# Performance work log

Hardware: AMD Instinct MI355X
Metric: run time of the kernel (lower is better)

Reference implementation:

```python
import jax, jax.numpy as jnp
import numpy as np

V = 32000      # vocab_size
CHI = 64       # bond_dim
PD = 64        # pos_dim
MAXLEN = 1024  # max_seq_len
B, T = 8, 512
LN_EPS = 1e-5


def setup_inputs() -> dict:
    key = jax.random.key(0)
    ks = jax.random.split(key, 8)
    return {
        "input_ids": jax.random.randint(ks[0], (B, T), 0, V),
        "target_ids": jax.random.randint(ks[1], (B, T), 0, V),
        # learned parameters (match torch init scales)
        "core": jax.random.normal(ks[2], (CHI, V, CHI), jnp.float32) * (1.0 / np.sqrt(CHI)),
        "h0": jax.random.normal(ks[3], (CHI,), jnp.float32) * 0.01,
        "pos_embed": jax.random.normal(ks[4], (MAXLEN, PD), jnp.float32) * 0.02,
        # mod_mlp: Linear(PD, 2*PD) -> GELU -> Linear(2*PD, 2*CHI), xavier gain=0.1, zero bias
        "W1": jax.random.normal(ks[5], (PD, 2 * PD), jnp.float32) * (0.1 * np.sqrt(6.0 / (PD + 2 * PD)) / np.sqrt(3.0)),
        "b1": jnp.zeros((2 * PD,), jnp.float32),
        "W2": jax.random.normal(ks[6], (2 * PD, 2 * CHI), jnp.float32) * (0.1 * np.sqrt(6.0 / (2 * PD + 2 * CHI)) / np.sqrt(3.0)),
        "b2": jnp.zeros((2 * CHI,), jnp.float32),
        "output_bias": jnp.zeros((V,), jnp.float32),
        "ln_gamma": jnp.ones((CHI,), jnp.float32),
        "ln_beta": jnp.zeros((CHI,), jnp.float32),
    }


def reference(input_ids, target_ids, core, h0, pos_embed, W1, b1, W2, b2,
              output_bias, ln_gamma, ln_beta):
    Bb, Tt = input_ids.shape
    chi = core.shape[0]

    # position modulation factors for positions 0..T-1
    pos_emb = pos_embed[:Tt]                                  # (T, PD)
    hmid = jax.nn.gelu(pos_emb @ W1 + b1, approximate=False)  # (T, 2*PD)
    mod = hmid @ W2 + b2                                      # (T, 2*CHI)
    ml, mr = jnp.split(mod, 2, axis=-1)
    ml = 1.0 + 0.5 * jnp.tanh(ml)                             # (T, chi)
    mr = 1.0 + 0.5 * jnp.tanh(mr)                             # (T, chi)

    def layer_norm(x):
        mu = jnp.mean(x, axis=-1, keepdims=True)
        var = jnp.var(x, axis=-1, keepdims=True)
        return (x - mu) * jax.lax.rsqrt(var + LN_EPS) * ln_gamma + ln_beta

    def step(h, xs):
        ml_t, mr_t, x_t = xs                                   # (chi,), (chi,), (B,)
        h_mod = h * ml_t                                       # (B, chi)
        # logits_t[b,v] = sum_ij h_mod[b,i] core[i,v,j] mr[j]
        core_r = jnp.einsum('ivj,j->iv', core, mr_t)           # (chi, V)
        logits_t = h_mod @ core_r + output_bias                # (B, V)
        # transition: h_new[b,j] = sum_i h_mod[b,i] core[i,x_b,j] mr[j]
        slices = core[:, x_t, :].transpose(1, 0, 2)            # (B, chi, chi)
        h_new = jnp.einsum('bi,bij->bj', h_mod, slices) * mr_t
        h_new = layer_norm(h_new)
        return h_new, logits_t

    h_init = jnp.broadcast_to(h0, (Bb, chi))
    _, logits = jax.lax.scan(step, h_init, (ml, mr, input_ids.T))  # (T, B, V)

    logits = logits.transpose(1, 0, 2).reshape(-1, logits.shape[-1]).astype(jnp.float32)
    targets = target_ids.reshape(-1)
    logp = jax.nn.log_softmax(logits, axis=-1)
    loss = -jnp.mean(jnp.take_along_axis(logp, targets[:, None], axis=1))
    return loss
```

## Files before the change

### kernel.cpp

```cpp
#include <hip/hip_runtime.h>
#include <math.h>

#define V 32000
#define T 512
#define NB 8
#define LN_EPS 1e-5f

typedef __attribute__((ext_vector_type(8))) short short8;
typedef __attribute__((ext_vector_type(4))) float f32x4;

__device__ __forceinline__ unsigned short f2b(float x) {
    unsigned int u = __float_as_uint(x);
    unsigned int r = (u + 0x7fffu + ((u >> 16) & 1u)) >> 16;
    return (unsigned short)r;
}
__device__ __forceinline__ float b2f(unsigned short h) {
    return __uint_as_float(((unsigned int)h) << 16);
}
__device__ __forceinline__ unsigned int pack_rn(float a, float b) {
    unsigned int ua = __float_as_uint(a) + 0x8000u;
    unsigned int ub = __float_as_uint(b) + 0x8000u;
    return __builtin_amdgcn_perm(ub, ua, 0x07060302u);
}

__global__ void k_mod(const float* __restrict__ pos, const float* __restrict__ W1,
                      const float* __restrict__ b1, const float* __restrict__ W2,
                      const float* __restrict__ b2, float* __restrict__ ml,
                      float* __restrict__ mr, unsigned short* __restrict__ mrb) {
    int t = blockIdx.x, tid = threadIdx.x;
    __shared__ float pos_s[64];
    __shared__ float hm_s[128];
    if (tid < 64) pos_s[tid] = pos[t * 64 + tid];
    __syncthreads();
    float acc = b1[tid];
#pragma unroll
    for (int p = 0; p < 64; p++) acc += pos_s[p] * W1[p * 128 + tid];
    float g = acc * 0.5f * (1.0f + erff(acc * 0.70710678118654752f));
    hm_s[tid] = g;
    __syncthreads();
    float acc2 = b2[tid];
#pragma unroll
    for (int k = 0; k < 128; k++) acc2 += hm_s[k] * W2[k * 128 + tid];
    float val = 1.0f + 0.5f * tanhf(acc2);
    if (tid < 64) ml[t * 64 + tid] = val;
    else { int c = tid - 64; mr[t * 64 + c] = val; mrb[t * 64 + c] = f2b(val); }
}

__global__ void __launch_bounds__(256) k_gather(const int* __restrict__ ids,
                                                const float* __restrict__ core,
                                                unsigned int* __restrict__ g) {
    int bt = blockIdx.x;
    int b = bt >> 9, t = bt & 511;
    int x = ids[b * T + t];
    unsigned int* dst = g + (size_t)bt * 2048;
#pragma unroll
    for (int e = 0; e < 2; e++) {
        int k = (e * 256 + threadIdx.x) * 4;
        int i2 = k >> 6, j = k & 63;
        f32x4 a = *reinterpret_cast<const f32x4*>(core + ((size_t)(2 * i2) * V + x) * 64 + j);
        f32x4 c = *reinterpret_cast<const f32x4*>(core + ((size_t)(2 * i2 + 1) * V + x) * 64 + j);
        uint4 o;
        o.x = pack_rn(a.x, c.x);
        o.y = pack_rn(a.y, c.y);
        o.z = pack_rn(a.z, c.z);
        o.w = pack_rn(a.w, c.w);
        *reinterpret_cast<uint4*>(dst + k) = o;
    }
}

__global__ void __launch_bounds__(64) k_scan(
    const unsigned int* __restrict__ g, const float* __restrict__ h0,
    const float* __restrict__ ml, const float* __restrict__ mr,
    const float* __restrict__ gam, const float* __restrict__ bet,
    unsigned short* __restrict__ hmod) {
    const int b = blockIdx.x, j = threadIdx.x;
    __shared__ float hm_s[64];
    float h = h0[j];
    const float gj = gam[j], bj = bet[j];
    const unsigned int* gb = g + (size_t)b * (512 * 2048);
    unsigned int B0[32], B1[32], B2[32], B3[32];
#pragma unroll
    for (int i = 0; i < 32; i++) B0[i] = gb[i * 64 + j];
#pragma unroll
    for (int i = 0; i < 32; i++) B1[i] = gb[2048 + i * 64 + j];

#define SCAN_BODY(TT, USE, PF)                                                \
    {                                                                         \
        int tp = (TT) + 2; if (tp > T - 1) tp = T - 1;                        \
        const unsigned int* gp = gb + (size_t)tp * 2048;                      \
        _Pragma("unroll")                                                     \
        for (int i = 0; i < 32; i++) PF[i] = gp[i * 64 + j];                  \
        float hmj = h * ml[(TT) * 64 + j];                                    \
        hmod[((TT) * 8 + b) * 64 + j] = f2b(hmj);                             \
        hm_s[j] = hmj;                                                        \
        asm volatile("s_waitcnt lgkmcnt(0)" ::: "memory");                    \
        float s0a = 0.f, s1a = 0.f, s0b = 0.f, s1b = 0.f;                     \
        _Pragma("unroll")                                                     \
        for (int i = 0; i < 16; i++) {                                        \
            unsigned int u = USE[i];                                          \
            s0a += __uint_as_float(u << 16) * hm_s[2 * i];                    \
            s1a += __uint_as_float(u & 0xffff0000u) * hm_s[2 * i + 1];        \
        }                                                                     \
        _Pragma("unroll")                                                     \
        for (int i = 16; i < 32; i++) {                                       \
            unsigned int u = USE[i];                                          \
            s0b += __uint_as_float(u << 16) * hm_s[2 * i];                    \
            s1b += __uint_as_float(u & 0xffff0000u) * hm_s[2 * i + 1];        \
        }                                                                     \
        float y = ((s0a + s0b) + (s1a + s1b)) * mr[(TT) * 64 + j];            \
        float sum = y, sq = y * y;                                            \
        _Pragma("unroll")                                                     \
        for (int m = 1; m < 64; m <<= 1) {                                    \
            sum += __shfl_xor(sum, m, 64);                                    \
            sq  += __shfl_xor(sq, m, 64);                                     \
        }                                                                     \
        float mu = sum * (1.f / 64.f);                                        \
        float var = sq * (1.f / 64.f) - mu * mu;                              \
        h = (y - mu) * rsqrtf(var + LN_EPS) * gj + bj;                        \
    }

    for (int t = 0; t < T; t += 4) {
        SCAN_BODY(t, B0, B2)
        SCAN_BODY(t + 1, B1, B3)
        SCAN_BODY(t + 2, B2, B0)
        SCAN_BODY(t + 3, B3, B1)
    }
#undef SCAN_BODY
}

#define BAR_LDS() do {                                             \
        asm volatile("s_waitcnt lgkmcnt(0)" ::: "memory");         \
        __builtin_amdgcn_s_barrier();                              \
    } while (0)

__global__ void __launch_bounds__(512, 4) k_logits(
    const float* __restrict__ core, const unsigned short* __restrict__ mrb,
    const unsigned short* __restrict__ hmod, const float* __restrict__ obias,
    const int* __restrict__ tgt, unsigned int* __restrict__ ws_ms,
    float* __restrict__ ws_tgt) {
    __shared__ __attribute__((aligned(16))) unsigned short r3s[8 * 2312];

    const int tid = threadIdx.x;
    const int w = tid >> 6;
    const int lane = tid & 63;
    const int q = lane >> 4;
    const int l15 = lane & 15;
    const int bx = blockIdx.x;
    const int v0 = bx * 8;
    const int myv = v0 + w;

    short8 cf[8];
#pragma unroll
    for (int it = 0; it < 4; it++) {
        const float* p = core + (((size_t)(it * 16 + l15)) * V + myv) * 64;
#pragma unroll
        for (int ks = 0; ks < 2; ks++) {
            f32x4 x0 = *reinterpret_cast<const f32x4*>(p + ks * 32 + q * 8);
            f32x4 x1 = *reinterpret_cast<const f32x4*>(p + ks * 32 + q * 8 + 4);
            union { short8 s; unsigned int u[4]; } pk;
            pk.u[0] = pack_rn(x0.x, x0.y);
            pk.u[1] = pack_rn(x0.z, x0.w);
            pk.u[2] = pack_rn(x1.x, x1.y);
            pk.u[3] = pack_rn(x1.z, x1.w);
            cf[it * 2 + ks] = pk.s;
        }
    }
    float biasv[4];
#pragma unroll
    for (int r = 0; r < 4; r++) biasv[r] = obias[v0 + (q & 1) * 4 + r];

    for (int ch = 0; ch < 16; ch++) {
        const int t0 = ch * 32;
#pragma unroll
        for (int tt = 0; tt < 2; tt++) {
            const int trow = t0 + tt * 16 + l15;
            short8 mf0 = *reinterpret_cast<const short8*>(mrb + trow * 64 + q * 8);
            short8 mf1 = *reinterpret_cast<const short8*>(mrb + trow * 64 + 32 + q * 8);
#pragma unroll
            for (int it = 0; it < 4; it++) {
                f32x4 acc = {0.f, 0.f, 0.f, 0.f};
                acc = __builtin_amdgcn_mfma_f32_16x16x32_bf16(cf[it * 2], mf0, acc, 0, 0, 0);
                acc = __builtin_amdgcn_mfma_f32_16x16x32_bf16(cf[it * 2 + 1], mf1, acc, 0, 0, 0);
                uint2 dd;
                dd.x = pack_rn(acc.x, acc.y);
                dd.y = pack_rn(acc.z, acc.w);
                *reinterpret_cast<uint2*>(
                    &r3s[w * 2312 + (tt * 16 + l15) * 72 + it * 16 + q * 4]) = dd;
            }
        }
        BAR_LDS();
        const int bb = l15 & 7;
        const int vp = (l15 & 7) * 2312;
#pragma unroll
        for (int e = 0; e < 4; e++) {
            const int tl = w * 4 + e;
            const int t = t0 + tl;
            short8 ra0 = *reinterpret_cast<const short8*>(&r3s[vp + tl * 72 + q * 8]);
            short8 ra1 = *reinterpret_cast<const short8*>(&r3s[vp + tl * 72 + 32 + q * 8]);
            short8 hb0 = *reinterpret_cast<const short8*>(hmod + ((size_t)t * 8 + bb) * 64 + q * 8);
            short8 hb1 = *reinterpret_cast<const short8*>(hmod + ((size_t)t * 8 + bb) * 64 + 32 + q * 8);
            f32x4 acc = {0.f, 0.f, 0.f, 0.f};
            acc = __builtin_amdgcn_mfma_f32_16x16x32_bf16(ra0, hb0, acc, 0, 0, 0);
            acc = __builtin_amdgcn_mfma_f32_16x16x32_bf16(ra1, hb1, acc, 0, 0, 0);
            float vals[4];
#pragma unroll
            for (int r = 0; r < 4; r++) vals[r] = acc[r] + biasv[r];
            if (q < 2 && l15 < 8) {
                int tg = tgt[bb * T + t];
#pragma unroll
                for (int r = 0; r < 4; r++)
                    if (tg == v0 + q * 4 + r) ws_tgt[l15 * T + t] = vals[r];
            }
            float m4 = fmaxf(fmaxf(vals[0], vals[1]), fmaxf(vals[2], vals[3]));
            float s4 = __expf(vals[0] - m4) + __expf(vals[1] - m4) +
                       __expf(vals[2] - m4) + __expf(vals[3] - m4);
            float om = __shfl_xor(m4, 16, 64);
            float os = __shfl_xor(s4, 16, 64);
            float mm = fmaxf(m4, om);
            float mq = b2f(f2b(mm));
            float ss = s4 * __expf(m4 - mq) + os * __expf(om - mq);
            if (q == 0 && l15 < 8) {
                ws_ms[(size_t)bx * 4096 + l15 * T + t] =
                    ((unsigned int)f2b(mq) << 16) | f2b(ss);
            }
        }
        BAR_LDS();
    }
}

__global__ void k_red1(const unsigned int* __restrict__ ws_ms,
                       float* __restrict__ o_m, float* __restrict__ o_s) {
    int bt = blockIdx.x * 256 + threadIdx.x;
    int kg = blockIdx.y;
    float m = -1e30f, s = 0.f;
    for (int kk = 0; kk < 100; kk++) {
        unsigned int pp = ws_ms[(size_t)(kg * 100 + kk) * 4096 + bt];
        float mk = b2f((unsigned short)(pp >> 16));
        float sk = b2f((unsigned short)(pp & 0xffff));
        float m2 = fmaxf(m, mk);
        s = s * __expf(m - m2) + sk * __expf(mk - m2);
        m = m2;
    }
    o_m[kg * 4096 + bt] = m; o_s[kg * 4096 + bt] = s;
}

__global__ void k_red2(const float* __restrict__ o_m, const float* __restrict__ o_s,
                       const float* __restrict__ wtgt, float* __restrict__ out) {
    int bt = blockIdx.x * 256 + threadIdx.x;
    float m = -1e30f, s = 0.f;
    for (int kg = 0; kg < 40; kg++) {
        float mk = o_m[kg * 4096 + bt], sk = o_s[kg * 4096 + bt];
        float m2 = fmaxf(m, mk);
        s = s * __expf(m - m2) + sk * __expf(mk - m2);
        m = m2;
    }
    float term = m + logf(s) - wtgt[bt];
    __shared__ float red[256];
    red[threadIdx.x] = term;
    __syncthreads();
    for (int st = 128; st > 0; st >>= 1) {
        if (threadIdx.x < st) red[threadIdx.x] += red[threadIdx.x + st];
        __syncthreads();
    }
    if (threadIdx.x == 0) atomicAdd(out, red[0] * (1.f / 4096.f));
}

extern "C" void kernel_launch(void* const* d_in, const int* in_sizes, int n_in,
                              void* d_out, int out_size, void* d_ws, size_t ws_size,
                              hipStream_t stream) {
    const int*   ids   = (const int*)d_in[0];
    const int*   tgt   = (const int*)d_in[1];
    const float* core  = (const float*)d_in[2];
    const float* h0    = (const float*)d_in[3];
    const float* pos   = (const float*)d_in[4];
    const float* W1    = (const float*)d_in[5];
    const float* b1    = (const float*)d_in[6];
    const float* W2    = (const float*)d_in[7];
    const float* b2    = (const float*)d_in[8];
    const float* obias = (const float*)d_in[9];
    const float* gam   = (const float*)d_in[10];
    const float* bet   = (const float*)d_in[11];

    char* ws = (char*)d_ws;
    float*          ws_ml  = (float*)(ws + 0);
    float*          ws_mr  = (float*)(ws + 131072);
    unsigned short* ws_mrb = (unsigned short*)(ws + 262144);
    unsigned short* ws_hm  = (unsigned short*)(ws + 327680);
    float*          ws_tg  = (float*)(ws + 851968);
    unsigned int*   g      = (unsigned int*)(ws + 868352);
    unsigned int*   ws_ms  = (unsigned int*)(ws + 868352);
    float*          o2m    = (float*)(ws + 66404352);
    float*          o2s    = (float*)(ws + 67059712);

    hipMemsetAsync(d_out, 0, sizeof(float), stream);

    k_mod<<<512, 128, 0, stream>>>(pos, W1, b1, W2, b2, ws_ml, ws_mr, ws_mrb);
    k_gather<<<4096, 256, 0, stream>>>(ids, core, g);
    k_scan<<<NB, 64, 0, stream>>>(g, h0, ws_ml, ws_mr, gam, bet, ws_hm);
    k_logits<<<4000, 512, 0, stream>>>(core, ws_mrb, ws_hm, obias, tgt, ws_ms, ws_tg);
    k_red1<<<dim3(16, 40), 256, 0, stream>>>(ws_ms, o2m, o2s);
    k_red2<<<16, 256, 0, stream>>>(o2m, o2s, ws_tg, (float*)d_out);
}
```

Before: 1.948 ms.

## Double-buffer LDS in logits kernel and use all lanes in second-stage MFMA

Splits the shared-memory staging buffer into two halves so that the first MFMA stage for the next 32-timestep chunk can run while the second stage consumes the previous chunk, cutting one barrier per chunk. The second stage is also remapped so the upper half of each 16-lane group handles a second timestep, halving the per-wave MFMA iterations from four to two. This doubles LDS use per block, which may reduce occupancy at 4 blocks per CU.

```diff
diff --git a/kernel.cpp b/kernel.cpp
--- a/kernel.cpp
+++ b/kernel.cpp
@@ -138,7 +138,7 @@
     const unsigned short* __restrict__ hmod, const float* __restrict__ obias,
     const int* __restrict__ tgt, unsigned int* __restrict__ ws_ms,
     float* __restrict__ ws_tgt) {
-    __shared__ __attribute__((aligned(16))) unsigned short r3s[8 * 2312];
+    __shared__ __attribute__((aligned(16))) unsigned short r3s[2][8 * 2312];
 
     const int tid = threadIdx.x;
     const int w = tid >> 6;
@@ -148,6 +148,11 @@
     const int bx = blockIdx.x;
     const int v0 = bx * 8;
     const int myv = v0 + w;
+    const int half = l15 >> 3;
+    const int bb = l15 & 7;
+    const int vp = bb * 2312;
+    const bool vrow_ok = ((q >> 1) == half);
+    const bool writer = (q == 2 * half);
 
     short8 cf[8];
 #pragma unroll
@@ -169,63 +174,80 @@
 #pragma unroll
     for (int r = 0; r < 4; r++) biasv[r] = obias[v0 + (q & 1) * 4 + r];
 
-    for (int ch = 0; ch < 16; ch++) {
-        const int t0 = ch * 32;
-#pragma unroll
-        for (int tt = 0; tt < 2; tt++) {
-            const int trow = t0 + tt * 16 + l15;
-            short8 mf0 = *reinterpret_cast<const short8*>(mrb + trow * 64 + q * 8);
-            short8 mf1 = *reinterpret_cast<const short8*>(mrb + trow * 64 + 32 + q * 8);
-#pragma unroll
-            for (int it = 0; it < 4; it++) {
-                f32x4 acc = {0.f, 0.f, 0.f, 0.f};
-                acc = __builtin_amdgcn_mfma_f32_16x16x32_bf16(cf[it * 2], mf0, acc, 0, 0, 0);
-                acc = __builtin_amdgcn_mfma_f32_16x16x32_bf16(cf[it * 2 + 1], mf1, acc, 0, 0, 0);
-                uint2 dd;
-                dd.x = pack_rn(acc.x, acc.y);
-                dd.y = pack_rn(acc.z, acc.w);
-                *reinterpret_cast<uint2*>(
-                    &r3s[w * 2312 + (tt * 16 + l15) * 72 + it * 16 + q * 4]) = dd;
-            }
-        }
+#define STAGE_A(T0v, BUF)                                                     \
+    {                                                                         \
+        const int t0a_ = (T0v);                                               \
+        _Pragma("unroll")                                                     \
+        for (int tt = 0; tt < 2; tt++) {                                      \
+            const int trow = t0a_ + tt * 16 + l15;                            \
+            short8 mf0 = *reinterpret_cast<const short8*>(mrb + trow * 64 + q * 8); \
+            short8 mf1 = *reinterpret_cast<const short8*>(mrb + trow * 64 + 32 + q * 8); \
+            _Pragma("unroll")                                                 \
+            for (int it = 0; it < 4; it++) {                                  \
+                f32x4 acc = {0.f, 0.f, 0.f, 0.f};                             \
+                acc = __builtin_amdgcn_mfma_f32_16x16x32_bf16(cf[it * 2], mf0, acc, 0, 0, 0); \
+                acc = __builtin_amdgcn_mfma_f32_16x16x32_bf16(cf[it * 2 + 1], mf1, acc, 0, 0, 0); \
+                uint2 dd;                                                     \
+                dd.x = pack_rn(acc.x, acc.y);                                 \
+                dd.y = pack_rn(acc.z, acc.w);                                 \
+                *reinterpret_cast<uint2*>(                                    \
+                    &r3s[BUF][w * 2312 + (tt * 16 + l15) * 72 + it * 16 + q * 4]) = dd; \
+            }                                                                 \
+        }                                                                     \
+    }
+
+#define STAGE_B(T0v, BUF)                                                     \
+    {                                                                         \
+        const int t0b_ = (T0v);                                               \
+        _Pragma("unroll")                                                     \
+        for (int p_ = 0; p_ < 2; p_++) {                                      \
+            const int tl_ = w * 4 + 2 * p_ + half;                            \
+            const int tb_ = t0b_ + tl_;                                       \
+            const unsigned short* hp_ = hmod + ((size_t)tb_ * 8 + bb) * 64 + q * 8; \
+            short8 hb0_ = *reinterpret_cast<const short8*>(hp_);              \
+            short8 hb1_ = *reinterpret_cast<const short8*>(hp_ + 32);         \
+            short8 ra0_ = *reinterpret_cast<const short8*>(&r3s[BUF][vp + tl_ * 72 + q * 8]); \
+            short8 ra1_ = *reinterpret_cast<const short8*>(&r3s[BUF][vp + tl_ * 72 + 32 + q * 8]); \
+            f32x4 acc_ = {0.f, 0.f, 0.f, 0.f};                                \
+            acc_ = __builtin_amdgcn_mfma_f32_16x16x32_bf16(ra0_, hb0_, acc_, 0, 0, 0); \
+            acc_ = __builtin_amdgcn_mfma_f32_16x16x32_bf16(ra1_, hb1_, acc_, 0, 0, 0); \
+            float vals_[4];                                                   \
+            _Pragma("unroll")                                                 \
+            for (int r = 0; r < 4; r++) vals_[r] = acc_[r] + biasv[r];        \
+            if (vrow_ok) {                                                    \
+                int tg_ = tgt[bb * T + tb_];                                  \
+                _Pragma("unroll")                                             \
+                for (int r = 0; r < 4; r++)                                   \
+                    if (tg_ == v0 + (q & 1) * 4 + r) ws_tgt[bb * T + tb_] = vals_[r]; \
+            }                                                                 \
+            float m4_ = fmaxf(fmaxf(vals_[0], vals_[1]), fmaxf(vals_[2], vals_[3])); \
+            float s4_ = __expf(vals_[0] - m4_) + __expf(vals_[1] - m4_) +     \
+                        __expf(vals_[2] - m4_) + __expf(vals_[3] - m4_);      \
+            float om_ = __shfl_xor(m4_, 16, 64);                              \
+            float os_ = __shfl_xor(s4_, 16, 64);                              \
+            float mm_ = fmaxf(m4_, om_);                                      \
+            float mq_ = b2f(f2b(mm_));                                        \
+            float ss_ = s4_ * __expf(m4_ - mq_) + os_ * __expf(om_ - mq_);    \
+            if (writer) {                                                     \
+                ws_ms[(size_t)bx * 4096 + bb * T + tb_] =                     \
+                    ((unsigned int)f2b(mq_) << 16) | f2b(ss_);                \
+            }                                                                 \
+        }                                                                     \
+    }
+
+    STAGE_A(0, 0);
+    BAR_LDS();
+#pragma unroll 1
+    for (int ch = 0; ch < 16; ch += 2) {
+        STAGE_A((ch + 1) * 32, 1);
+        STAGE_B(ch * 32, 0);
         BAR_LDS();
-        const int bb = l15 & 7;
-        const int vp = (l15 & 7) * 2312;
-#pragma unroll
-        for (int e = 0; e < 4; e++) {
-            const int tl = w * 4 + e;
-            const int t = t0 + tl;
-            short8 ra0 = *reinterpret_cast<const short8*>(&r3s[vp + tl * 72 + q * 8]);
-            short8 ra1 = *reinterpret_cast<const short8*>(&r3s[vp + tl * 72 + 32 + q * 8]);
-            short8 hb0 = *reinterpret_cast<const short8*>(hmod + ((size_t)t * 8 + bb) * 64 + q * 8);
-            short8 hb1 = *reinterpret_cast<const short8*>(hmod + ((size_t)t * 8 + bb) * 64 + 32 + q * 8);
-            f32x4 acc = {0.f, 0.f, 0.f, 0.f};
-            acc = __builtin_amdgcn_mfma_f32_16x16x32_bf16(ra0, hb0, acc, 0, 0, 0);
-            acc = __builtin_amdgcn_mfma_f32_16x16x32_bf16(ra1, hb1, acc, 0, 0, 0);
-            float vals[4];
-#pragma unroll
-            for (int r = 0; r < 4; r++) vals[r] = acc[r] + biasv[r];
-            if (q < 2 && l15 < 8) {
-                int tg = tgt[bb * T + t];
-#pragma unroll
-                for (int r = 0; r < 4; r++)
-                    if (tg == v0 + q * 4 + r) ws_tgt[l15 * T + t] = vals[r];
-            }
-            float m4 = fmaxf(fmaxf(vals[0], vals[1]), fmaxf(vals[2], vals[3]));
-            float s4 = __expf(vals[0] - m4) + __expf(vals[1] - m4) +
-                       __expf(vals[2] - m4) + __expf(vals[3] - m4);
-            float om = __shfl_xor(m4, 16, 64);
-            float os = __shfl_xor(s4, 16, 64);
-            float mm = fmaxf(m4, om);
-            float mq = b2f(f2b(mm));
-            float ss = s4 * __expf(m4 - mq) + os * __expf(om - mq);
-            if (q == 0 && l15 < 8) {
-                ws_ms[(size_t)bx * 4096 + l15 * T + t] =
-                    ((unsigned int)f2b(mq) << 16) | f2b(ss);
-            }
-        }
+        if (ch + 2 < 16) STAGE_A((ch + 2) * 32, 0);
+        STAGE_B((ch + 1) * 32, 1);
         BAR_LDS();
     }
+#undef STAGE_A
+#undef STAGE_B
 }
 
 __global__ void k_red1(const unsigned int* __restrict__ ws_ms,
```

Measured after the change: 1.687 ms. -13.4%, faster.
